# Optimization experiments

Hardware: AMD Instinct MI355X
Metric: run time of the kernel (lower is better)

Reference implementation:

```python
import jax, jax.numpy as jnp
import numpy as np

D_MODEL = 1024
N_QK = 32
D_QK = 32
N_OV = 2048
D_OV = 1
SEQ = 1024
BATCH = 2
VKV = 16
ROT_DIM = 32
ROT_BASE = 10000.0
SCALE = D_QK ** 0.5  # cfg.attn_scale default = sqrt(d_qk_head)


def _kaiming(k, shape, fan_in):
    # torch kaiming_normal_(mode='fan_in', nonlinearity='relu'): std = sqrt(2/fan_in)
    return jax.random.normal(k, shape, jnp.float32) * np.sqrt(2.0 / fan_in)


def setup_inputs() -> dict:
    key = jax.random.key(0)
    ks = jax.random.split(key, 7)
    return {
        'resid': jax.random.normal(ks[0], (BATCH, SEQ, D_MODEL), jnp.float32),
        'W_Q': _kaiming(ks[1], (N_QK, D_MODEL, D_QK), D_MODEL * D_QK),
        'W_K': _kaiming(ks[2], (N_QK, D_MODEL, D_QK), D_MODEL * D_QK),
        'W_V': _kaiming(ks[3], (N_OV, D_MODEL, D_OV), D_MODEL * D_OV),
        'W_O': _kaiming(ks[4], (N_OV, D_OV, D_MODEL), D_OV * D_MODEL),
        'b_Q': jnp.zeros((N_QK, D_QK), jnp.float32),
        'b_K': jnp.zeros((N_QK, D_QK), jnp.float32),
        'b_V': jnp.zeros((N_OV, D_OV), jnp.float32),
        'virtual_k': _kaiming(ks[5], (VKV, N_QK, D_QK), N_QK * D_QK),
        'virtual_v': jnp.zeros((VKV, N_OV, D_OV), jnp.float32),
    }


def _rotary_sin_cos(n_ctx, rd, base):
    # GPT-NeoX style (non-adjacent pairs): freq repeated as (2 d)
    pos = jnp.arange(n_ctx, dtype=jnp.float32)
    dim = jnp.arange(rd // 2, dtype=jnp.float32)
    freq = base ** (dim / (rd / 2))
    freq = jnp.concatenate([freq, freq])
    angles = pos[:, None] / freq[None, :]  # (n_ctx, rd)
    return jnp.sin(angles), jnp.cos(angles)


def _apply_rotary(x, sin, cos, rd):
    # x: (batch, seq, head, d_head)
    s = x.shape[1]
    x_rot, x_pass = x[..., :rd], x[..., rd:]
    flip = jnp.concatenate([-x_rot[..., rd // 2:], x_rot[..., :rd // 2]], axis=-1)
    rot = x_rot * cos[None, :s, None, :] + flip * sin[None, :s, None, :]
    return jnp.concatenate([rot, x_pass], axis=-1)


def reference(resid, W_Q, W_K, W_V, W_O, b_Q, b_K, b_V, virtual_k, virtual_v):
    b, s, _ = resid.shape
    # per-head QKV projections + biases
    q = jnp.einsum('bsm,hmd->bshd', resid, W_Q) + b_Q  # (b,s,n_qk,d_qk)
    k = jnp.einsum('bsm,hmd->bshd', resid, W_K) + b_K
    v = jnp.einsum('bsm,hmd->bshd', resid, W_V) + b_V  # (b,s,n_ov,d_ov)
    sin, cos = _rotary_sin_cos(s, ROT_DIM, ROT_BASE)
    q = _apply_rotary(q, sin, cos, ROT_DIM)
    k = _apply_rotary(k, sin, cos, ROT_DIM)
    # append virtual KV at the end of the key axis
    k = jnp.concatenate([k, jnp.broadcast_to(virtual_k[None], (b,) + virtual_k.shape)], axis=1)
    v = jnp.concatenate([v, jnp.broadcast_to(virtual_v[None], (b,) + virtual_v.shape)], axis=1)
    kv_len = s + VKV
    scores = jnp.einsum('bqhd,bkhd->bhqk', q, k) / SCALE
    # causal mask: tril(ones(n_ctx, n_ctx+vkv), diagonal=vkv)
    mask = jnp.arange(kv_len)[None, :] <= (jnp.arange(s)[:, None] + VKV)
    scores = jnp.where(mask[None, None], scores, -jnp.inf)
    pattern = jax.nn.softmax(scores, axis=-1)
    pattern = jnp.where(jnp.isnan(pattern), 0.0, pattern)
    # repeat_interleave of pattern over ov heads == grouping v per qk head
    ratio = N_OV // N_QK
    v_g = v.reshape(b, kv_len, N_QK, ratio * D_OV)
    z = jnp.einsum('bhqk,bkhr->bqhr', pattern, v_g)  # (b,s,n_qk,ratio*d_ov)
    z = z.reshape(b, s, N_OV, D_OV)
    out = jnp.einsum('bqhd,hdm->bqm', z, W_O)  # cal_out: no b_O
    return out
```

## Files before the change

kernel.cpp:

```cpp
#include <hip/hip_runtime.h>
#include <hip/hip_bf16.h>
#include <math.h>


typedef short bf16x8 __attribute__((ext_vector_type(8)));
typedef short short4v __attribute__((ext_vector_type(4)));
typedef float f32x4 __attribute__((ext_vector_type(4)));
typedef int int4v __attribute__((ext_vector_type(4)));
typedef __hip_bfloat16 bf16;

#define AS1(p) ((const __attribute__((address_space(1))) void*)(const void*)(p))
#define AS3(p) ((__attribute__((address_space(3))) void*)(void*)(p))

static constexpr float INV_SCALE = 0.17677669529663687f;

__device__ inline short rnd_bf16(float x) {
  unsigned u = __float_as_uint(x);
  return (short)((u + 0x7fffu + ((u >> 16) & 1u)) >> 16);
}

__device__ inline int pack_bf16_pair(float hi, float lo) {
  unsigned a = __float_as_uint(hi) + 0x8000u;
  unsigned b = __float_as_uint(lo) + 0x8000u;
  return (int)__builtin_amdgcn_perm(a, b, 0x07060302u);
}

__global__ __launch_bounds__(256) void prep(
    const float* __restrict__ resid, const float* __restrict__ WV,
    const float* __restrict__ WQ, const float* __restrict__ WK,
    const float* __restrict__ WO, const float* __restrict__ vk,
    const float* __restrict__ vv,
    bf16* __restrict__ A_bf, bf16* __restrict__ Wt, bf16* __restrict__ Wot,
    bf16* __restrict__ Kb, bf16* __restrict__ Vb) {
  __shared__ float t[64][65];
  const int blk = blockIdx.x, tid = threadIdx.x;
  if (blk < 4096) {
    const float* src = (blk < 2048) ? resid : WV;
    short* dst = (short*)((blk < 2048) ? A_bf : (Wt + (size_t)2048 * 1024));
    int i = ((blk & 2047) * 256 + tid) * 4;
    float4 v = *(const float4*)(src + i);
    dst[i + 0] = rnd_bf16(v.x); dst[i + 1] = rnd_bf16(v.y);
    dst[i + 2] = rnd_bf16(v.z); dst[i + 3] = rnd_bf16(v.w);
  } else if (blk < 7168) {
    int idx = (blk - 4096) * 256 + tid;
    if (idx < 262144) {
      int b = idx >> 17, rem = idx & 131071;
      int j = rem >> 10, c = rem & 1023;
      int h = c >> 5, d = c & 31;
      float v = (j < 16) ? vk[j * 1024 + c] : 0.f;
      Kb[(((size_t)(b * 32 + h)) * 1152 + 1024 + j) * 32 + d] = __float2bfloat16(v);
    } else if (idx < 524288) {
      int i2 = idx - 262144;
      int b = i2 >> 17, rem = i2 & 131071;
      int ch = rem >> 6, p = rem & 63;
      int pl = p & 31;
      int u = (p & 32) | ((pl & 4) << 2) | ((pl & 24) >> 1) | (pl & 3);
      float v = (u < 16) ? vv[(size_t)u * 2048 + ch] : 0.f;
      int hv = ch >> 6, c = ch & 63;
      int slot = c * 8 + ((p >> 3) ^ (c & 7));
      Vb[((((size_t)(b * 32 + hv)) * 17 + 16) * 512 + slot) * 8 + (p & 7)] = __float2bfloat16(v);
    }
  } else if (blk < 8192) {
    int i = blk - 7168;
    int mt = i & 15, h = (i >> 4) & 31, qk = i >> 9;
    const float* W = qk ? WK : WQ;
    const int m0 = mt * 64;
    for (int idx = tid; idx < 64 * 32; idx += 256) {
      int ii = idx >> 5, d = idx & 31;
      t[ii][d] = W[((size_t)h * 1024 + m0 + ii) * 32 + d];
    }
    __syncthreads();
    const int rowbase = qk * 1024 + h * 32;
    for (int idx = tid; idx < 32 * 64; idx += 256) {
      int d = idx >> 6, ii = idx & 63;
      Wt[(size_t)(rowbase + d) * 1024 + m0 + ii] = __float2bfloat16(t[ii][d]);
    }
  } else {
    int i = blk - 8192;
    int h0 = (i & 31) * 64, m0 = (i >> 5) * 64;
    for (int idx = tid; idx < 64 * 64; idx += 256) {
      int ii = idx >> 6, j = idx & 63;
      t[ii][j] = WO[(size_t)(h0 + ii) * 1024 + m0 + j];
    }
    __syncthreads();
    for (int idx = tid; idx < 64 * 64; idx += 256) {
      int ii = idx >> 6, j = idx & 63;
      Wot[(size_t)(m0 + ii) * 2048 + h0 + j] = __float2bfloat16(t[j][ii]);
    }
  }
}

__global__ __launch_bounds__(256) void gemm1_fused(
    const bf16* __restrict__ A, const bf16* __restrict__ Bt,
    const float* __restrict__ bQ, const float* __restrict__ bK,
    const float* __restrict__ bV,
    bf16* __restrict__ Qb, bf16* __restrict__ Kb, bf16* __restrict__ Vb) {
  __shared__ __align__(16) short As[128 * 128];
  __shared__ __align__(16) short Bs[128 * 128];
  const int flat = blockIdx.x;
  const int xcd = flat & 7, idx = flat >> 3;
  const int tileM = (xcd * 2 + (idx >> 5)) * 128;
  const int tileN = (idx & 31) * 128;
  const int tid = threadIdx.x, wave = tid >> 6, lane = tid & 63;
  const int wm = (wave >> 1) * 64, wn = (wave & 1) * 64;
  const int mrow = lane & 15, kq = lane >> 4;
  const bool isQK = tileN < 2048;
  f32x4 acc[4][4] = {};

  for (int k0 = 0; k0 < 1024; k0 += 128) {
#pragma unroll
    for (int i = 0; i < 8; i++) {
      int c = (wave * 8 + i) * 64 + lane;
      int row = c >> 4, j = c & 15, g = j ^ (row & 15);
      const short* ga = (const short*)A + (size_t)(tileM + row) * 1024 + k0 + g * 8;
      const short* gb = (const short*)Bt + (size_t)(tileN + row) * 1024 + k0 + g * 8;
      __builtin_amdgcn_global_load_lds(AS1(ga), AS3(&As[(wave * 8 + i) * 512]), 16, 0, 0);
      __builtin_amdgcn_global_load_lds(AS1(gb), AS3(&Bs[(wave * 8 + i) * 512]), 16, 0, 0);
    }
    __syncthreads();
#pragma unroll
    for (int ks = 0; ks < 4; ks++) {
      bf16x8 af[4], bfr[4];
#pragma unroll
      for (int t = 0; t < 4; t++) {
        int ra = wm + t * 16 + mrow, rb = wn + t * 16 + mrow;
        af[t]  = *(const bf16x8*)&As[ra * 128 + ((ks * 4 + kq) ^ (ra & 15)) * 8];
        bfr[t] = *(const bf16x8*)&Bs[rb * 128 + ((ks * 4 + kq) ^ (rb & 15)) * 8];
      }
      if (isQK) {
#pragma unroll
        for (int fj = 0; fj < 4; fj++)
#pragma unroll
          for (int ti = 0; ti < 4; ti++)
            acc[fj][ti] = __builtin_amdgcn_mfma_f32_16x16x32_bf16(bfr[fj], af[ti], acc[fj][ti], 0, 0, 0);
      } else {
#pragma unroll
        for (int i = 0; i < 4; i++)
#pragma unroll
          for (int j = 0; j < 4; j++)
            acc[i][j] = __builtin_amdgcn_mfma_f32_16x16x32_bf16(af[i], bfr[j], acc[i][j], 0, 0, 0);
      }
    }
    __syncthreads();
  }

  const int col = lane & 15, rq = lane >> 4;
  if (isQK) {
    const int qk = tileN >> 10;
    const float* bias = qk ? bK : bQ;
    const int hA = ((tileN & 1023) + wn) >> 5;
    const int d0 = rq * 4;
    const float4 bA0 = *(const float4*)&bias[hA * 32 + d0];
    const float4 bA1 = *(const float4*)&bias[hA * 32 + 16 + d0];
    const float4 bB0 = *(const float4*)&bias[(hA + 1) * 32 + d0];
    const float4 bB1 = *(const float4*)&bias[(hA + 1) * 32 + 16 + d0];
    float invf[4];
#pragma unroll
    for (int r = 0; r < 4; r++)
      invf[r] = exp2f((d0 + r) * -0.8304820237218406f);
    const float osc = qk ? 1.f : INV_SCALE;
#pragma unroll
    for (int ti = 0; ti < 4; ti++) {
      int sg = tileM + wm + ti * 16 + col;
      int s = sg & 1023, bb = sg >> 10;
      float sv[4], cv[4];
#pragma unroll
      for (int r = 0; r < 4; r++) __sincosf((float)s * invf[r], &sv[r], &cv[r]);
#pragma unroll
      for (int p = 0; p < 2; p++) {
        int h = hA + p;
        short4v z0, z1;
#pragma unroll
        for (int r = 0; r < 4; r++) {
          float x0 = acc[2 * p][ti][r]     + (p ? (&bB0.x)[r] : (&bA0.x)[r]);
          float x1 = acc[2 * p + 1][ti][r] + (p ? (&bB1.x)[r] : (&bA1.x)[r]);
          float y0 = (x0 * cv[r] - x1 * sv[r]) * osc;
          float y1 = (x1 * cv[r] + x0 * sv[r]) * osc;
          z0[r] = rnd_bf16(y0); z1[r] = rnd_bf16(y1);
        }
        short* dst = qk
            ? (short*)Kb + ((size_t)(bb * 32 + h) * 1152 + s) * 32
            : (short*)Qb + ((size_t)(bb * 32 + h) * 1024 + s) * 32;
        *(short4v*)(dst + d0) = z0;
        *(short4v*)(dst + 16 + d0) = z1;
      }
    }
  } else {
    const int hv = (tileN - 2048 + wn) >> 6;
#pragma unroll
    for (int i = 0; i < 4; i++)
#pragma unroll
      for (int j = 0; j < 4; j++) {
        int c = j * 16 + col;
        float bias = bV[hv * 64 + c];
        int m0 = tileM + wm + i * 16 + rq * 4;
        int s0 = m0 & 1023, bb = m0 >> 10;
        int chunk = s0 >> 6, w = s0 & 63, u0 = w & 31;
        int p0 = (u0 & 3) | ((u0 & 16) >> 2) | ((u0 & 8) << 1) | ((u0 & 4) << 1);
        int p = (w & 32) | p0;
        int slot = c * 8 + ((p >> 3) ^ (c & 7));
        short4v s4;
#pragma unroll
        for (int r = 0; r < 4; r++) s4[r] = rnd_bf16(acc[i][j][r] + bias);
        *(short4v*)((short*)Vb +
            ((((size_t)(bb * 32 + hv)) * 17 + chunk) * 512 + slot) * 8 + (p & 7)) = s4;
      }
  }
}

__global__ __launch_bounds__(256) void attn_mfma(
    const bf16* __restrict__ Qb, const bf16* __restrict__ Kb,
    const bf16* __restrict__ Vb, bf16* __restrict__ Zb) {
  __shared__ __align__(16) short Vs[4][2][4096];
  const int flat = blockIdx.x;
  const int xcd = flat & 7;
  const int hqb = xcd * 8 + ((flat >> 3) & 7);
  const int xb = flat >> 6;
  const int xblk = (xb < 4) ? xb : (11 - xb);
  const int hq = hqb & 31, b = hqb >> 5;
  const int wave = threadIdx.x >> 6, lane = threadIdx.x & 63;
  const int col = lane & 15, quad = lane >> 4;
  const int pairIdx = xblk * 4 + wave;
  const int qwA = pairIdx * 16, qwB = (63 - pairIdx) * 16;

  const short* qbase = (const short*)Qb + ((size_t)(b * 32 + hq)) * 1024 * 32;
  const bf16x8 qfA = *(const bf16x8*)(qbase + (qwA + col) * 32 + quad * 8);
  const bf16x8 qfB = *(const bf16x8*)(qbase + (qwB + col) * 32 + quad * 8);
  const short* kbase = (const short*)Kb + ((size_t)(b * 32 + hq)) * 1152 * 32 + quad * 8;
  const short* vbh = (const short*)Vb + ((size_t)(b * 32 + hq)) * (17 * 4096) + lane * 8;

  const int kendA = qwA + 32;
  const int nchA = (kendA + 63) >> 6;
  const int kendB = (qwB + 32 < 1040) ? qwB + 32 : 1040;
  const int nchB = (kendB + 63) >> 6;

  f32x4 OA[4] = {}, OB[4] = {};
  float lsA = 0.f, lsB = 0.f;

  bf16x8 kf[4];
#pragma unroll
  for (int mbk = 0; mbk < 4; mbk++)
    kf[mbk] = *(const bf16x8*)(kbase + (size_t)(mbk * 16 + col) * 32);
  {
    short* vd = &Vs[wave][0][0];
#pragma unroll
    for (int g = 0; g < 8; g++)
      __builtin_amdgcn_global_load_lds(AS1(vbh + g * 512), AS3(vd + g * 512), 16, 0, 0);
  }

  for (int ci = 0; ci < nchB; ci++) {
    const int kc = ci * 64;
    const bool aAct = ci < nchA;
    __builtin_amdgcn_s_setprio(1);
    f32x4 SB[4] = {};
#pragma unroll
    for (int mbk = 0; mbk < 4; mbk++)
      SB[mbk] = __builtin_amdgcn_mfma_f32_16x16x32_bf16(kf[mbk], qfB, SB[mbk], 0, 0, 0);
    f32x4 SA[4] = {};
    if (aAct) {
#pragma unroll
      for (int mbk = 0; mbk < 4; mbk++)
        SA[mbk] = __builtin_amdgcn_mfma_f32_16x16x32_bf16(kf[mbk], qfA, SA[mbk], 0, 0, 0);
    }
    __builtin_amdgcn_s_setprio(0);
    if (kc + 63 > qwB + 16) {
      int qv = qwB + col + 16;
#pragma unroll
      for (int mbk = 0; mbk < 4; mbk++)
#pragma unroll
        for (int r = 0; r < 4; r++)
          if (kc + mbk * 16 + quad * 4 + r > qv) SB[mbk][r] = -1e30f;
    }
    if (aAct && kc + 63 > qwA + 16) {
      int qv = qwA + col + 16;
#pragma unroll
      for (int mbk = 0; mbk < 4; mbk++)
#pragma unroll
        for (int r = 0; r < 4; r++)
          if (kc + mbk * 16 + quad * 4 + r > qv) SA[mbk][r] = -1e30f;
    }
    int4v piB[2], piA[2];
    {
#pragma unroll
      for (int mbk = 0; mbk < 4; mbk++)
#pragma unroll
        for (int r = 0; r < 4; r++) {
          float p = __expf(SB[mbk][r]);
          lsB += p;
          SB[mbk][r] = p;
        }
#pragma unroll
      for (int pr = 0; pr < 2; pr++)
#pragma unroll
        for (int d = 0; d < 4; d++)
          piB[pr][d] = pack_bf16_pair(SB[2 * pr + (d >> 1)][(d & 1) * 2 + 1],
                                      SB[2 * pr + (d >> 1)][(d & 1) * 2]);
    }
    if (aAct) {
#pragma unroll
      for (int mbk = 0; mbk < 4; mbk++)
#pragma unroll
        for (int r = 0; r < 4; r++) {
          float p = __expf(SA[mbk][r]);
          lsA += p;
          SA[mbk][r] = p;
        }
#pragma unroll
      for (int pr = 0; pr < 2; pr++)
#pragma unroll
        for (int d = 0; d < 4; d++)
          piA[pr][d] = pack_bf16_pair(SA[2 * pr + (d >> 1)][(d & 1) * 2 + 1],
                                      SA[2 * pr + (d >> 1)][(d & 1) * 2]);
    }
    asm volatile("s_waitcnt vmcnt(0)" ::: "memory");
    const short* vd = &Vs[wave][ci & 1][0];
    bf16x8 vf[2][4];
#pragma unroll
    for (int ks = 0; ks < 2; ks++)
#pragma unroll
      for (int cb = 0; cb < 4; cb++) {
        int slot = (cb * 16 + col) * 8 + ((ks * 4 + quad) ^ (col & 7));
        vf[ks][cb] = *(const bf16x8*)(vd + slot * 8);
      }
    if (ci + 1 < nchB) {
      const int kn = kc + 64;
#pragma unroll
      for (int mbk = 0; mbk < 4; mbk++)
        kf[mbk] = *(const bf16x8*)(kbase + (size_t)(kn + mbk * 16 + col) * 32);
      const short* vsrc = vbh + (ci + 1) * 4096;
      short* vdn = &Vs[wave][(ci + 1) & 1][0];
#pragma unroll
      for (int g = 0; g < 8; g++)
        __builtin_amdgcn_global_load_lds(AS1(vsrc + g * 512), AS3(vdn + g * 512), 16, 0, 0);
    }
    __builtin_amdgcn_s_setprio(1);
#pragma unroll
    for (int ks = 0; ks < 2; ks++) {
      bf16x8 prB = *(bf16x8*)&piB[ks];
#pragma unroll
      for (int cb = 0; cb < 4; cb++)
        OB[cb] = __builtin_amdgcn_mfma_f32_16x16x32_bf16(vf[ks][cb], prB, OB[cb], 0, 0, 0);
    }
    if (aAct) {
#pragma unroll
      for (int ks = 0; ks < 2; ks++) {
        bf16x8 prA = *(bf16x8*)&piA[ks];
#pragma unroll
        for (int cb = 0; cb < 4; cb++)
          OA[cb] = __builtin_amdgcn_mfma_f32_16x16x32_bf16(vf[ks][cb], prA, OA[cb], 0, 0, 0);
      }
    }
    __builtin_amdgcn_s_setprio(0);
  }
  lsA += __shfl_xor(lsA, 16);
  lsA += __shfl_xor(lsA, 32);
  lsB += __shfl_xor(lsB, 16);
  lsB += __shfl_xor(lsB, 32);
  {
    float inv = 1.f / lsA;
    short* zrow = (short*)Zb + ((size_t)(b * 1024 + qwA + col)) * 2048 + hq * 64 + quad * 4;
#pragma unroll
    for (int cb = 0; cb < 4; cb++) {
      short4v s4;
#pragma unroll
      for (int r = 0; r < 4; r++) s4[r] = rnd_bf16(OA[cb][r] * inv);
      *(short4v*)(zrow + cb * 16) = s4;
    }
  }
  {
    float inv = 1.f / lsB;
    short* zrow = (short*)Zb + ((size_t)(b * 1024 + qwB + col)) * 2048 + hq * 64 + quad * 4;
#pragma unroll
    for (int cb = 0; cb < 4; cb++) {
      short4v s4;
#pragma unroll
      for (int r = 0; r < 4; r++) s4[r] = rnd_bf16(OB[cb][r] * inv);
      *(short4v*)(zrow + cb * 16) = s4;
    }
  }
}

__global__ __launch_bounds__(256) void gemm2_small(
    const bf16* __restrict__ A, const bf16* __restrict__ Bt, float* __restrict__ C,
    int K, int ldc) {
  __shared__ __align__(16) short As[2][64 * 128];
  __shared__ __align__(16) short Bs[2][64 * 128];
  const int tileM = blockIdx.y * 64, tileN = blockIdx.x * 64;
  const int tid = threadIdx.x, wave = tid >> 6, lane = tid & 63;
  const int wm = (wave >> 1) * 32, wn = (wave & 1) * 32;
  const int mrow = lane & 15, kq = lane >> 4;
  f32x4 acc[2][2] = {};

  const int cbase = wave * 4;
  const int nt = K >> 7;

#define G2_STAGE(buf, k0)                                                     \
  {                                                                           \
    _Pragma("unroll")                                                         \
    for (int i = 0; i < 4; i++) {                                             \
      int c = (cbase + i) * 64 + lane;                                        \
      int row = c >> 4, j = c & 15, g = j ^ (row & 15);                       \
      const short* ga = (const short*)A + (size_t)(tileM + row) * K + (k0) + g * 8; \
      const short* gb = (const short*)Bt + (size_t)(tileN + row) * K + (k0) + g * 8; \
      __builtin_amdgcn_global_load_lds(AS1(ga), AS3(&As[buf][(cbase + i) * 512]), 16, 0, 0); \
      __builtin_amdgcn_global_load_lds(AS1(gb), AS3(&Bs[buf][(cbase + i) * 512]), 16, 0, 0); \
    }                                                                         \
  }

  G2_STAGE(0, 0);
  __syncthreads();
  int cur = 0;
  for (int t = 0; t < nt; ++t) {
    if (t + 1 < nt) G2_STAGE(cur ^ 1, (t + 1) << 7);
    const short* as = &As[cur][0];
    const short* bs = &Bs[cur][0];
#pragma unroll
    for (int ks = 0; ks < 4; ks++) {
      bf16x8 af[2], bfr[2];
#pragma unroll
      for (int t2 = 0; t2 < 2; t2++) {
        int ra = wm + t2 * 16 + mrow, rb = wn + t2 * 16 + mrow;
        af[t2]  = *(const bf16x8*)&as[ra * 128 + ((ks * 4 + kq) ^ (ra & 15)) * 8];
        bfr[t2] = *(const bf16x8*)&bs[rb * 128 + ((ks * 4 + kq) ^ (rb & 15)) * 8];
      }
#pragma unroll
      for (int i = 0; i < 2; i++)
#pragma unroll
        for (int j = 0; j < 2; j++)
          acc[i][j] = __builtin_amdgcn_mfma_f32_16x16x32_bf16(af[i], bfr[j], acc[i][j], 0, 0, 0);
    }
    __syncthreads();
    cur ^= 1;
  }
#undef G2_STAGE

  const int col = lane & 15, rq = lane >> 4;
#pragma unroll
  for (int i = 0; i < 2; i++)
#pragma unroll
    for (int j = 0; j < 2; j++)
#pragma unroll
      for (int r = 0; r < 4; r++) {
        int mm = tileM + wm + i * 16 + rq * 4 + r;
        int nn = tileN + wn + j * 16 + col;
        C[(size_t)mm * ldc + nn] = acc[i][j][r];
      }
}

extern "C" void kernel_launch(void* const* d_in, const int* in_sizes, int n_in,
                              void* d_out, int out_size, void* d_ws, size_t ws_size,
                              hipStream_t stream) {
  const float* resid = (const float*)d_in[0];
  const float* WQ = (const float*)d_in[1];
  const float* WK = (const float*)d_in[2];
  const float* WV = (const float*)d_in[3];
  const float* WO = (const float*)d_in[4];
  const float* bQ = (const float*)d_in[5];
  const float* bK = (const float*)d_in[6];
  const float* bV = (const float*)d_in[7];
  const float* vk = (const float*)d_in[8];
  const float* vv = (const float*)d_in[9];
  float* out = (float*)d_out;

  char* ws = (char*)d_ws;
  bf16* A_bf = (bf16*)(ws);
  bf16* Wt   = (bf16*)(ws + 4194304);
  bf16* Wot  = (bf16*)(ws + 12582912);
  bf16* Qb   = (bf16*)(ws + 16777216);
  bf16* Kb   = (bf16*)(ws + 20971520);
  bf16* Vb   = (bf16*)(ws + 25690112);
  bf16* Zb   = (bf16*)(ws + 35127296);

  prep<<<8704, 256, 0, stream>>>(resid, WV, WQ, WK, WO, vk, vv, A_bf, Wt, Wot, Kb, Vb);
  gemm1_fused<<<512, 256, 0, stream>>>(A_bf, Wt, bQ, bK, bV, Qb, Kb, Vb);
  attn_mfma<<<512, 256, 0, stream>>>(Qb, Kb, Vb, Zb);
  gemm2_small<<<dim3(16, 32), 256, 0, stream>>>(Zb, Wot, out, 2048, 1024);
}
```

Measured before the change: 153.3 us.

## Split attention query-tile pairs across separate waves and fold log2e into Q scale

The attention kernel now runs 512 threads per block, giving each of 8 waves one 16-row query tile instead of each of 4 waves handling a paired short and long tile. It single-buffers the V tile in LDS and adds an explicit lgkmcnt wait before prefetching into the same buffer. It also folds log2(e) into the Q scaling so the softmax can use the raw exp2 instruction. The aim is more waves for latency hiding and fewer live registers per wave. The trade-offs are waves with uneven work, since long and short tiles no longer share a wave, and loss of the V double buffering overlap.

```diff
diff --git a/kernel.cpp b/kernel.cpp
--- a/kernel.cpp
+++ b/kernel.cpp
@@ -13,6 +13,8 @@
 #define AS3(p) ((__attribute__((address_space(3))) void*)(void*)(p))
 
 static constexpr float INV_SCALE = 0.17677669529663687f;
+static constexpr float INV_SCALE_LG2E =
+    0.17677669529663687f * 1.4426950408889634f;
 
 __device__ inline short rnd_bf16(float x) {
   unsigned u = __float_as_uint(x);
@@ -158,7 +160,7 @@
 #pragma unroll
     for (int r = 0; r < 4; r++)
       invf[r] = exp2f((d0 + r) * -0.8304820237218406f);
-    const float osc = qk ? 1.f : INV_SCALE;
+    const float osc = qk ? 1.f : INV_SCALE_LG2E;
 #pragma unroll
     for (int ti = 0; ti < 4; ti++) {
       int sg = tileM + wm + ti * 16 + col;
@@ -208,10 +210,10 @@
   }
 }
 
-__global__ __launch_bounds__(256) void attn_mfma(
+__global__ __launch_bounds__(512, 4) void attn_mfma(
     const bf16* __restrict__ Qb, const bf16* __restrict__ Kb,
     const bf16* __restrict__ Vb, bf16* __restrict__ Zb) {
-  __shared__ __align__(16) short Vs[4][2][4096];
+  __shared__ __align__(16) short Vs[8][4096];
   const int flat = blockIdx.x;
   const int xcd = flat & 7;
   const int hqb = xcd * 8 + ((flat >> 3) & 7);
@@ -220,100 +222,61 @@
   const int hq = hqb & 31, b = hqb >> 5;
   const int wave = threadIdx.x >> 6, lane = threadIdx.x & 63;
   const int col = lane & 15, quad = lane >> 4;
-  const int pairIdx = xblk * 4 + wave;
-  const int qwA = pairIdx * 16, qwB = (63 - pairIdx) * 16;
+  const int pairIdx = xblk * 4 + (wave >> 1);
+  const int qw = (wave & 1) ? pairIdx * 16 : (63 - pairIdx) * 16;
 
   const short* qbase = (const short*)Qb + ((size_t)(b * 32 + hq)) * 1024 * 32;
-  const bf16x8 qfA = *(const bf16x8*)(qbase + (qwA + col) * 32 + quad * 8);
-  const bf16x8 qfB = *(const bf16x8*)(qbase + (qwB + col) * 32 + quad * 8);
+  const bf16x8 qf = *(const bf16x8*)(qbase + (qw + col) * 32 + quad * 8);
   const short* kbase = (const short*)Kb + ((size_t)(b * 32 + hq)) * 1152 * 32 + quad * 8;
   const short* vbh = (const short*)Vb + ((size_t)(b * 32 + hq)) * (17 * 4096) + lane * 8;
 
-  const int kendA = qwA + 32;
-  const int nchA = (kendA + 63) >> 6;
-  const int kendB = (qwB + 32 < 1040) ? qwB + 32 : 1040;
-  const int nchB = (kendB + 63) >> 6;
-
-  f32x4 OA[4] = {}, OB[4] = {};
-  float lsA = 0.f, lsB = 0.f;
+  const int kend = (qw + 32 < 1040) ? qw + 32 : 1040;
+  const int nch = (kend + 63) >> 6;
+
+  f32x4 O[4] = {};
+  float ls = 0.f;
 
   bf16x8 kf[4];
 #pragma unroll
   for (int mbk = 0; mbk < 4; mbk++)
     kf[mbk] = *(const bf16x8*)(kbase + (size_t)(mbk * 16 + col) * 32);
-  {
-    short* vd = &Vs[wave][0][0];
-#pragma unroll
-    for (int g = 0; g < 8; g++)
-      __builtin_amdgcn_global_load_lds(AS1(vbh + g * 512), AS3(vd + g * 512), 16, 0, 0);
-  }
-
-  for (int ci = 0; ci < nchB; ci++) {
+  short* vd = &Vs[wave][0];
+#pragma unroll
+  for (int g = 0; g < 8; g++)
+    __builtin_amdgcn_global_load_lds(AS1(vbh + g * 512), AS3(vd + g * 512), 16, 0, 0);
+
+  for (int ci = 0; ci < nch; ci++) {
     const int kc = ci * 64;
-    const bool aAct = ci < nchA;
     __builtin_amdgcn_s_setprio(1);
-    f32x4 SB[4] = {};
+    f32x4 S[4] = {};
 #pragma unroll
     for (int mbk = 0; mbk < 4; mbk++)
-      SB[mbk] = __builtin_amdgcn_mfma_f32_16x16x32_bf16(kf[mbk], qfB, SB[mbk], 0, 0, 0);
-    f32x4 SA[4] = {};
-    if (aAct) {
+      S[mbk] = __builtin_amdgcn_mfma_f32_16x16x32_bf16(kf[mbk], qf, S[mbk], 0, 0, 0);
+    __builtin_amdgcn_s_setprio(0);
+    if (kc + 63 > qw + 16) {
+      int qv = qw + col + 16;
 #pragma unroll
       for (int mbk = 0; mbk < 4; mbk++)
-        SA[mbk] = __builtin_amdgcn_mfma_f32_16x16x32_bf16(kf[mbk], qfA, SA[mbk], 0, 0, 0);
-    }
-    __builtin_amdgcn_s_setprio(0);
-    if (kc + 63 > qwB + 16) {
-      int qv = qwB + col + 16;
-#pragma unroll
-      for (int mbk = 0; mbk < 4; mbk++)
 #pragma unroll
         for (int r = 0; r < 4; r++)
-          if (kc + mbk * 16 + quad * 4 + r > qv) SB[mbk][r] = -1e30f;
-    }
-    if (aAct && kc + 63 > qwA + 16) {
-      int qv = qwA + col + 16;
-#pragma unroll
-      for (int mbk = 0; mbk < 4; mbk++)
-#pragma unroll
-        for (int r = 0; r < 4; r++)
-          if (kc + mbk * 16 + quad * 4 + r > qv) SA[mbk][r] = -1e30f;
-    }
-    int4v piB[2], piA[2];
-    {
-#pragma unroll
-      for (int mbk = 0; mbk < 4; mbk++)
-#pragma unroll
-        for (int r = 0; r < 4; r++) {
-          float p = __expf(SB[mbk][r]);
-          lsB += p;
-          SB[mbk][r] = p;
-        }
-#pragma unroll
-      for (int pr = 0; pr < 2; pr++)
-#pragma unroll
-        for (int d = 0; d < 4; d++)
-          piB[pr][d] = pack_bf16_pair(SB[2 * pr + (d >> 1)][(d & 1) * 2 + 1],
-                                      SB[2 * pr + (d >> 1)][(d & 1) * 2]);
-    }
-    if (aAct) {
-#pragma unroll
-      for (int mbk = 0; mbk < 4; mbk++)
-#pragma unroll
-        for (int r = 0; r < 4; r++) {
-          float p = __expf(SA[mbk][r]);
-          lsA += p;
-          SA[mbk][r] = p;
-        }
-#pragma unroll
-      for (int pr = 0; pr < 2; pr++)
-#pragma unroll
-        for (int d = 0; d < 4; d++)
-          piA[pr][d] = pack_bf16_pair(SA[2 * pr + (d >> 1)][(d & 1) * 2 + 1],
-                                      SA[2 * pr + (d >> 1)][(d & 1) * 2]);
-    }
+          if (kc + mbk * 16 + quad * 4 + r > qv) S[mbk][r] = -1e30f;
+    }
+    int4v pi[2];
+#pragma unroll
+    for (int mbk = 0; mbk < 4; mbk++)
+#pragma unroll
+      for (int r = 0; r < 4; r++) {
+        float p = __builtin_amdgcn_exp2f(S[mbk][r]);
+        ls += p;
+        S[mbk][r] = p;
+      }
+#pragma unroll
+    for (int pr = 0; pr < 2; pr++)
+#pragma unroll
+      for (int d = 0; d < 4; d++)
+        pi[pr][d] = pack_bf16_pair(S[2 * pr + (d >> 1)][(d & 1) * 2 + 1],
+                                   S[2 * pr + (d >> 1)][(d & 1) * 2]);
     asm volatile("s_waitcnt vmcnt(0)" ::: "memory");
-    const short* vd = &Vs[wave][ci & 1][0];
     bf16x8 vf[2][4];
 #pragma unroll
     for (int ks = 0; ks < 2; ks++)
@@ -322,59 +285,38 @@
         int slot = (cb * 16 + col) * 8 + ((ks * 4 + quad) ^ (col & 7));
         vf[ks][cb] = *(const bf16x8*)(vd + slot * 8);
       }
-    if (ci + 1 < nchB) {
+    asm volatile("s_waitcnt lgkmcnt(0)" ::: "memory");
+    __builtin_amdgcn_sched_barrier(0);
+    if (ci + 1 < nch) {
       const int kn = kc + 64;
 #pragma unroll
       for (int mbk = 0; mbk < 4; mbk++)
         kf[mbk] = *(const bf16x8*)(kbase + (size_t)(kn + mbk * 16 + col) * 32);
       const short* vsrc = vbh + (ci + 1) * 4096;
-      short* vdn = &Vs[wave][(ci + 1) & 1][0];
 #pragma unroll
       for (int g = 0; g < 8; g++)
-        __builtin_amdgcn_global_load_lds(AS1(vsrc + g * 512), AS3(vdn + g * 512), 16, 0, 0);
+        __builtin_amdgcn_global_load_lds(AS1(vsrc + g * 512), AS3(vd + g * 512), 16, 0, 0);
     }
     __builtin_amdgcn_s_setprio(1);
 #pragma unroll
     for (int ks = 0; ks < 2; ks++) {
-      bf16x8 prB = *(bf16x8*)&piB[ks];
+      bf16x8 pr = *(bf16x8*)&pi[ks];
 #pragma unroll
       for (int cb = 0; cb < 4; cb++)
-        OB[cb] = __builtin_amdgcn_mfma_f32_16x16x32_bf16(vf[ks][cb], prB, OB[cb], 0, 0, 0);
-    }
-    if (aAct) {
-#pragma unroll
-      for (int ks = 0; ks < 2; ks++) {
-        bf16x8 prA = *(bf16x8*)&piA[ks];
-#pragma unroll
-        for (int cb = 0; cb < 4; cb++)
-          OA[cb] = __builtin_amdgcn_mfma_f32_16x16x32_bf16(vf[ks][cb], prA, OA[cb], 0, 0, 0);
-      }
+        O[cb] = __builtin_amdgcn_mfma_f32_16x16x32_bf16(vf[ks][cb], pr, O[cb], 0, 0, 0);
     }
     __builtin_amdgcn_s_setprio(0);
   }
-  lsA += __shfl_xor(lsA, 16);
-  lsA += __shfl_xor(lsA, 32);
-  lsB += __shfl_xor(lsB, 16);
-  lsB += __shfl_xor(lsB, 32);
+  ls += __shfl_xor(ls, 16);
+  ls += __shfl_xor(ls, 32);
   {
-    float inv = 1.f / lsA;
-    short* zrow = (short*)Zb + ((size_t)(b * 1024 + qwA + col)) * 2048 + hq * 64 + quad * 4;
+    float inv = 1.f / ls;
+    short* zrow = (short*)Zb + ((size_t)(b * 1024 + qw + col)) * 2048 + hq * 64 + quad * 4;
 #pragma unroll
     for (int cb = 0; cb < 4; cb++) {
       short4v s4;
 #pragma unroll
-      for (int r = 0; r < 4; r++) s4[r] = rnd_bf16(OA[cb][r] * inv);
-      *(short4v*)(zrow + cb * 16) = s4;
-    }
-  }
-  {
-    float inv = 1.f / lsB;
-    short* zrow = (short*)Zb + ((size_t)(b * 1024 + qwB + col)) * 2048 + hq * 64 + quad * 4;
-#pragma unroll
-    for (int cb = 0; cb < 4; cb++) {
-      short4v s4;
-#pragma unroll
-      for (int r = 0; r < 4; r++) s4[r] = rnd_bf16(OB[cb][r] * inv);
+      for (int r = 0; r < 4; r++) s4[r] = rnd_bf16(O[cb][r] * inv);
       *(short4v*)(zrow + cb * 16) = s4;
     }
   }
@@ -473,6 +415,6 @@
 
   prep<<<8704, 256, 0, stream>>>(resid, WV, WQ, WK, WO, vk, vv, A_bf, Wt, Wot, Kb, Vb);
   gemm1_fused<<<512, 256, 0, stream>>>(A_bf, Wt, bQ, bK, bV, Qb, Kb, Vb);
-  attn_mfma<<<512, 256, 0, stream>>>(Qb, Kb, Vb, Zb);
+  attn_mfma<<<512, 512, 0, stream>>>(Qb, Kb, Vb, Zb);
   gemm2_small<<<dim3(16, 32), 256, 0, stream>>>(Zb, Wot, out, 2048, 1024);
 }
```

After: 158.3 us. 1.03x slower.

## Load V fragments directly from global memory and fold log2e into Q scale

Applied to the files above, without the earlier changes.

Removes the per-wave LDS double buffer for V, which was filled with global_load_lds and then read back. V fragments are now loaded straight from global memory into registers at the top of each chunk, using precomputed swizzled offsets. It also folds log2(e) into the Q scaling in the projection epilogue so softmax can use the raw exp2 instruction instead of __expf. This cuts LDS traffic and the vmcnt wait, but V loads are no longer prefetched a chunk ahead, so global latency may be more exposed.

```diff
diff --git a/kernel.cpp b/kernel.cpp
--- a/kernel.cpp
+++ b/kernel.cpp
@@ -13,6 +13,8 @@
 #define AS3(p) ((__attribute__((address_space(3))) void*)(void*)(p))
 
 static constexpr float INV_SCALE = 0.17677669529663687f;
+static constexpr float INV_SCALE_LG2E =
+    0.17677669529663687f * 1.4426950408889634f;
 
 __device__ inline short rnd_bf16(float x) {
   unsigned u = __float_as_uint(x);
@@ -158,7 +160,7 @@
 #pragma unroll
     for (int r = 0; r < 4; r++)
       invf[r] = exp2f((d0 + r) * -0.8304820237218406f);
-    const float osc = qk ? 1.f : INV_SCALE;
+    const float osc = qk ? 1.f : INV_SCALE_LG2E;
 #pragma unroll
     for (int ti = 0; ti < 4; ti++) {
       int sg = tileM + wm + ti * 16 + col;
@@ -211,7 +213,6 @@
 __global__ __launch_bounds__(256) void attn_mfma(
     const bf16* __restrict__ Qb, const bf16* __restrict__ Kb,
     const bf16* __restrict__ Vb, bf16* __restrict__ Zb) {
-  __shared__ __align__(16) short Vs[4][2][4096];
   const int flat = blockIdx.x;
   const int xcd = flat & 7;
   const int hqb = xcd * 8 + ((flat >> 3) & 7);
@@ -227,7 +228,14 @@
   const bf16x8 qfA = *(const bf16x8*)(qbase + (qwA + col) * 32 + quad * 8);
   const bf16x8 qfB = *(const bf16x8*)(qbase + (qwB + col) * 32 + quad * 8);
   const short* kbase = (const short*)Kb + ((size_t)(b * 32 + hq)) * 1152 * 32 + quad * 8;
-  const short* vbh = (const short*)Vb + ((size_t)(b * 32 + hq)) * (17 * 4096) + lane * 8;
+  const short* vbase = (const short*)Vb + ((size_t)(b * 32 + hq)) * (17 * 4096);
+
+  int voff[2][4];
+#pragma unroll
+  for (int ks = 0; ks < 2; ks++)
+#pragma unroll
+    for (int cb = 0; cb < 4; cb++)
+      voff[ks][cb] = ((cb * 16 + col) * 8 + ((ks * 4 + quad) ^ (col & 7))) * 8;
 
   const int kendA = qwA + 32;
   const int nchA = (kendA + 63) >> 6;
@@ -241,16 +249,17 @@
 #pragma unroll
   for (int mbk = 0; mbk < 4; mbk++)
     kf[mbk] = *(const bf16x8*)(kbase + (size_t)(mbk * 16 + col) * 32);
-  {
-    short* vd = &Vs[wave][0][0];
-#pragma unroll
-    for (int g = 0; g < 8; g++)
-      __builtin_amdgcn_global_load_lds(AS1(vbh + g * 512), AS3(vd + g * 512), 16, 0, 0);
-  }
 
   for (int ci = 0; ci < nchB; ci++) {
     const int kc = ci * 64;
     const bool aAct = ci < nchA;
+    const short* vchunk = vbase + ci * 4096;
+    bf16x8 vf[2][4];
+#pragma unroll
+    for (int ks = 0; ks < 2; ks++)
+#pragma unroll
+      for (int cb = 0; cb < 4; cb++)
+        vf[ks][cb] = *(const bf16x8*)(vchunk + voff[ks][cb]);
     __builtin_amdgcn_s_setprio(1);
     f32x4 SB[4] = {};
 #pragma unroll
@@ -280,28 +289,26 @@
           if (kc + mbk * 16 + quad * 4 + r > qv) SA[mbk][r] = -1e30f;
     }
     int4v piB[2], piA[2];
-    {
+#pragma unroll
+    for (int mbk = 0; mbk < 4; mbk++)
+#pragma unroll
+      for (int r = 0; r < 4; r++) {
+        float p = __builtin_amdgcn_exp2f(SB[mbk][r]);
+        lsB += p;
+        SB[mbk][r] = p;
+      }
+#pragma unroll
+    for (int pr = 0; pr < 2; pr++)
+#pragma unroll
+      for (int d = 0; d < 4; d++)
+        piB[pr][d] = pack_bf16_pair(SB[2 * pr + (d >> 1)][(d & 1) * 2 + 1],
+                                    SB[2 * pr + (d >> 1)][(d & 1) * 2]);
+    if (aAct) {
 #pragma unroll
       for (int mbk = 0; mbk < 4; mbk++)
 #pragma unroll
         for (int r = 0; r < 4; r++) {
-          float p = __expf(SB[mbk][r]);
-          lsB += p;
-          SB[mbk][r] = p;
-        }
-#pragma unroll
-      for (int pr = 0; pr < 2; pr++)
-#pragma unroll
-        for (int d = 0; d < 4; d++)
-          piB[pr][d] = pack_bf16_pair(SB[2 * pr + (d >> 1)][(d & 1) * 2 + 1],
-                                      SB[2 * pr + (d >> 1)][(d & 1) * 2]);
-    }
-    if (aAct) {
-#pragma unroll
-      for (int mbk = 0; mbk < 4; mbk++)
-#pragma unroll
-        for (int r = 0; r < 4; r++) {
-          float p = __expf(SA[mbk][r]);
+          float p = __builtin_amdgcn_exp2f(SA[mbk][r]);
           lsA += p;
           SA[mbk][r] = p;
         }
@@ -312,26 +319,11 @@
           piA[pr][d] = pack_bf16_pair(SA[2 * pr + (d >> 1)][(d & 1) * 2 + 1],
                                       SA[2 * pr + (d >> 1)][(d & 1) * 2]);
     }
-    asm volatile("s_waitcnt vmcnt(0)" ::: "memory");
-    const short* vd = &Vs[wave][ci & 1][0];
-    bf16x8 vf[2][4];
-#pragma unroll
-    for (int ks = 0; ks < 2; ks++)
-#pragma unroll
-      for (int cb = 0; cb < 4; cb++) {
-        int slot = (cb * 16 + col) * 8 + ((ks * 4 + quad) ^ (col & 7));
-        vf[ks][cb] = *(const bf16x8*)(vd + slot * 8);
-      }
     if (ci + 1 < nchB) {
       const int kn = kc + 64;
 #pragma unroll
       for (int mbk = 0; mbk < 4; mbk++)
         kf[mbk] = *(const bf16x8*)(kbase + (size_t)(kn + mbk * 16 + col) * 32);
-      const short* vsrc = vbh + (ci + 1) * 4096;
-      short* vdn = &Vs[wave][(ci + 1) & 1][0];
-#pragma unroll
-      for (int g = 0; g < 8; g++)
-        __builtin_amdgcn_global_load_lds(AS1(vsrc + g * 512), AS3(vdn + g * 512), 16, 0, 0);
     }
     __builtin_amdgcn_s_setprio(1);
 #pragma unroll
```

Measured after the change: 154.7 us. About the same (+1.0%).
